# Kernel optimization log

Hardware: AMD Instinct MI355X
Metric: run time of the kernel (lower is better)

Reference implementation:

```python
import jax, jax.numpy as jnp
import numpy as np

TEMPERATURE = 0.5
EPS = 1e-8  # matches torch CosineSimilarity eps


def setup_inputs() -> dict:
    key = jax.random.key(0)
    k1, k2 = jax.random.split(key)
    N, D = 4096, 256
    z1 = jax.random.normal(k1, (N, D), dtype=jnp.float32)
    z2 = jax.random.normal(k2, (N, D), dtype=jnp.float32)
    return {"z1": z1, "z2": z2}


def reference(z1, z2):
    N = z1.shape[0]
    z = jnp.concatenate([z1, z2], axis=0)            # [2N, D]
    norm = jnp.linalg.norm(z, axis=-1, keepdims=True)
    zn = z / jnp.maximum(norm, EPS)                  # L2-normalized
    sim = (zn @ zn.T) / TEMPERATURE                  # [2N, 2N] cosine sim / temp
    # mask self-similarity on the diagonal
    diag = jnp.eye(2 * N, dtype=bool)
    sim = jnp.where(diag, -jnp.inf, sim)
    # positive pair labels: row i pairs with i+N (first half) or i-N (second half)
    labels = jnp.concatenate([jnp.arange(N) + N, jnp.arange(N)])
    logp = jax.nn.log_softmax(sim, axis=-1)
    loss = -jnp.mean(logp[jnp.arange(2 * N), labels])
    return loss
```

## Files before the change

### kernel.cpp

```cpp
#include <hip/hip_runtime.h>
#include <hip/hip_bf16.h>


#define NROWS 8192
#define NHALF 4096
#define DDIM  256

typedef __bf16 bf16;
typedef __bf16 bf16x4 __attribute__((ext_vector_type(4)));
typedef __bf16 bf16x8 __attribute__((ext_vector_type(8)));
typedef float  f32x4  __attribute__((ext_vector_type(4)));

__constant__ const float kTwoLog2e = 2.8853900817779268f;
__constant__ const float kLn2      = 0.6931471805599453f;

__device__ __forceinline__ const float* zrow(const float* z1, const float* z2, int r) {
  return (r < NHALF) ? (z1 + (size_t)r * DDIM) : (z2 + (size_t)(r - NHALF) * DDIM);
}

__global__ void k_normalize(const float* __restrict__ z1, const float* __restrict__ z2,
                            bf16* __restrict__ zn, float* __restrict__ invn,
                            float* __restrict__ rowsum) {
  const int wave = threadIdx.x >> 6, lane = threadIdx.x & 63;
  const int row = blockIdx.x * 4 + wave;
  const float* src = zrow(z1, z2, row);
  f32x4 v = *(const f32x4*)(src + lane * 4);
  float ss = v.x * v.x + v.y * v.y + v.z * v.z + v.w * v.w;
#pragma unroll
  for (int off = 1; off < 64; off <<= 1) ss += __shfl_xor(ss, off);
  const float inv = 1.0f / fmaxf(sqrtf(ss), 1e-8f);
  bf16x4 o;
  o.x = (bf16)(v.x * inv); o.y = (bf16)(v.y * inv);
  o.z = (bf16)(v.z * inv); o.w = (bf16)(v.w * inv);
  *(bf16x4*)(zn + (size_t)row * DDIM + lane * 4) = o;
  if (lane == 0) { invn[row] = inv; rowsum[row] = 0.0f; }
}

#define BM 256
#define BN 64
#define CSPLIT 8
#define LDSB 528

__global__ __launch_bounds__(512, 2) void k_gram(const bf16* __restrict__ zn,
                                                 float* __restrict__ rowsum) {
  __shared__ __align__(16) unsigned char lds[2][BN * LDSB];
  const int tid  = threadIdx.x;
  const int wave = tid >> 6, lane = tid & 63;
  const int quad = lane >> 4, l15 = lane & 15;
  const int rowblk = blockIdx.x >> 3, csplit = blockIdx.x & 7;
  const int c0 = csplit * (NROWS / CSPLIT);
  const int iters = (NROWS / CSPLIT) / BN;

  bf16x8 a[2][8];
#pragma unroll
  for (int s = 0; s < 2; ++s) {
    const int row = rowblk * BM + wave * 32 + s * 16 + l15;
    const bf16x8* ap = (const bf16x8*)(zn + (size_t)row * DDIM);
#pragma unroll
    for (int k = 0; k < 8; ++k) a[s][k] = ap[k * 4 + quad];
  }

  const int tr = tid >> 3;
  const int tc = tid & 7;

  uint4 g[4];
  {
    const unsigned char* gp = (const unsigned char*)(zn + (size_t)(c0 + tr) * DDIM);
#pragma unroll
    for (int j = 0; j < 4; ++j) g[j] = *(const uint4*)(gp + (tc + 8 * j) * 16);
  }
#pragma unroll
  for (int j = 0; j < 4; ++j)
    *(uint4*)(&lds[0][tr * LDSB + (tc + 8 * j) * 16]) = g[j];

  float sum[2][4] = {{0.f, 0.f, 0.f, 0.f}, {0.f, 0.f, 0.f, 0.f}};
  const f32x4 zero4 = {0.f, 0.f, 0.f, 0.f};

  for (int it = 0; it < iters; ++it) {
    __syncthreads();
    const int cur = it & 1;
    if (it + 1 < iters) {
      const unsigned char* gp =
          (const unsigned char*)(zn + (size_t)(c0 + (it + 1) * BN + tr) * DDIM);
#pragma unroll
      for (int j = 0; j < 4; ++j) g[j] = *(const uint4*)(gp + (tc + 8 * j) * 16);
    }

    f32x4 acc[2][4];
#pragma unroll
    for (int s = 0; s < 2; ++s)
#pragma unroll
      for (int cs = 0; cs < 4; ++cs) acc[s][cs] = zero4;

#pragma unroll
    for (int k = 0; k < 8; ++k) {
      bf16x8 b[4];
#pragma unroll
      for (int cs = 0; cs < 4; ++cs)
        b[cs] = *(const bf16x8*)(&lds[cur][(cs * 16 + l15) * LDSB + k * 64 + quad * 16]);
#pragma unroll
      for (int s = 0; s < 2; ++s)
#pragma unroll
        for (int cs = 0; cs < 4; ++cs)
          acc[s][cs] = __builtin_amdgcn_mfma_f32_16x16x32_bf16(a[s][k], b[cs], acc[s][cs], 0, 0, 0);
    }

#pragma unroll
    for (int s = 0; s < 2; ++s)
#pragma unroll
      for (int cs = 0; cs < 4; ++cs)
#pragma unroll
        for (int r = 0; r < 4; ++r)
          sum[s][r] += __builtin_amdgcn_exp2f(acc[s][cs][r] * kTwoLog2e);

    if (it + 1 < iters) {
#pragma unroll
      for (int j = 0; j < 4; ++j)
        *(uint4*)(&lds[(it + 1) & 1][tr * LDSB + (tc + 8 * j) * 16]) = g[j];
    }
  }

#pragma unroll
  for (int s = 0; s < 2; ++s)
#pragma unroll
    for (int r = 0; r < 4; ++r) {
      float v = sum[s][r];
      v += __shfl_xor(v, 1); v += __shfl_xor(v, 2);
      v += __shfl_xor(v, 4); v += __shfl_xor(v, 8);
      if (l15 == 0) {
        const int row = rowblk * BM + wave * 32 + s * 16 + quad * 4 + r;
        atomicAdd(&rowsum[row], v);
      }
    }
}

__global__ void k_finalize(const float* __restrict__ z1, const float* __restrict__ z2,
                           const bf16* __restrict__ zn, const float* __restrict__ invn,
                           const float* __restrict__ rowsum, float* __restrict__ contrib) {
  const int wave = threadIdx.x >> 6, lane = threadIdx.x & 63;
  const int row = blockIdx.x * 4 + wave;
  const int pr = (row < NHALF) ? row + NHALF : row - NHALF;

  f32x4 a4 = *(const f32x4*)(zrow(z1, z2, row) + lane * 4);
  f32x4 b4 = *(const f32x4*)(zrow(z1, z2, pr) + lane * 4);
  bf16x4 nb = *(const bf16x4*)(zn + (size_t)row * DDIM + lane * 4);

  float pd = a4.x * b4.x + a4.y * b4.y + a4.z * b4.z + a4.w * b4.w;
  float f0 = (float)nb.x, f1 = (float)nb.y, f2 = (float)nb.z, f3 = (float)nb.w;
  float nd = f0 * f0 + f1 * f1 + f2 * f2 + f3 * f3;
#pragma unroll
  for (int off = 1; off < 64; off <<= 1) {
    pd += __shfl_xor(pd, off);
    nd += __shfl_xor(nd, off);
  }
  if (lane == 0) {
    const float p = 2.0f * pd * invn[row] * invn[pr];
    const float dexp = __builtin_amdgcn_exp2f(kTwoLog2e * nd);
    const float lse = __builtin_amdgcn_logf(rowsum[row] - dexp) * kLn2;
    contrib[row] = lse - p;
  }
}

__global__ void k_reduce(const float* __restrict__ contrib, float* __restrict__ out) {
  const int wave = threadIdx.x >> 6, lane = threadIdx.x & 63;
  float acc = 0.0f;
  for (int i = threadIdx.x; i < NROWS; i += 256) acc += contrib[i];
#pragma unroll
  for (int off = 1; off < 64; off <<= 1) acc += __shfl_xor(acc, off);
  __shared__ float wsum[4];
  if (lane == 0) wsum[wave] = acc;
  __syncthreads();
  if (threadIdx.x == 0)
    out[0] = (wsum[0] + wsum[1] + wsum[2] + wsum[3]) * (1.0f / (float)NROWS);
}

extern "C" void kernel_launch(void* const* d_in, const int* in_sizes, int n_in,
                              void* d_out, int out_size, void* d_ws, size_t ws_size,
                              hipStream_t stream) {
  const float* z1 = (const float*)d_in[0];
  const float* z2 = (const float*)d_in[1];
  unsigned char* ws = (unsigned char*)d_ws;

  bf16* zn = (bf16*)ws;
  float* invn = (float*)(ws + (size_t)NROWS * DDIM * sizeof(bf16));
  float* rowsum = invn + NROWS;
  float* contrib = rowsum + NROWS;

  hipLaunchKernelGGL(k_normalize, dim3(NROWS / 4), dim3(256), 0, stream, z1, z2, zn, invn, rowsum);
  hipLaunchKernelGGL(k_gram, dim3((NROWS / BM) * CSPLIT), dim3(512), 0, stream, zn, rowsum);
  hipLaunchKernelGGL(k_finalize, dim3(NROWS / 4), dim3(256), 0, stream, z1, z2, zn, invn, rowsum,
                     contrib);
  hipLaunchKernelGGL(k_reduce, dim3(1), dim3(256), 0, stream, contrib, (float*)d_out);
}
```

Measured before the change: 107.6 us.

## Exploit Gram symmetry with upper-triangular tiles and fold temperature scaling into operands

The Gram kernel now computes only upper-triangular 128x128 tiles and adds each off-diagonal tile's exponentials into both the row sums and, through LDS column sums, the transposed row sums. That roughly halves the MFMA and exp work. The 2*log2e scale is folded into one bf16 copy of the normalized rows, which removes the per-element multiply. The finalize and reduce kernels are merged into one kernel that accumulates into the output with atomics, dropping a launch. In exchange, the positive-pair dot now uses the bf16 values instead of fp32, there is extra atomic traffic, and the triangular index decode is a serial loop.

```diff
diff --git a/kernel.cpp b/kernel.cpp
--- a/kernel.cpp
+++ b/kernel.cpp
@@ -5,85 +5,91 @@
 #define NROWS 8192
 #define NHALF 4096
 #define DDIM  256
+#define GT    128
+#define NTILES (NROWS / GT)
+#define NBLK  (NTILES * (NTILES + 1) / 2)
+#define BN    64
+#define LDSB  528
 
 typedef __bf16 bf16;
 typedef __bf16 bf16x4 __attribute__((ext_vector_type(4)));
 typedef __bf16 bf16x8 __attribute__((ext_vector_type(8)));
 typedef float  f32x4  __attribute__((ext_vector_type(4)));
 
-__constant__ const float kTwoLog2e = 2.8853900817779268f;
-__constant__ const float kLn2      = 0.6931471805599453f;
-
-__device__ __forceinline__ const float* zrow(const float* z1, const float* z2, int r) {
-  return (r < NHALF) ? (z1 + (size_t)r * DDIM) : (z2 + (size_t)(r - NHALF) * DDIM);
-}
+__constant__ const float kC   = 2.8853900817779268f;
+__constant__ const float kLn2 = 0.6931471805599453f;
 
 __global__ void k_normalize(const float* __restrict__ z1, const float* __restrict__ z2,
-                            bf16* __restrict__ zn, float* __restrict__ invn,
-                            float* __restrict__ rowsum) {
+                            bf16* __restrict__ znA, bf16* __restrict__ znB,
+                            float* __restrict__ rowsum, float* __restrict__ out) {
   const int wave = threadIdx.x >> 6, lane = threadIdx.x & 63;
   const int row = blockIdx.x * 4 + wave;
-  const float* src = zrow(z1, z2, row);
+  const float* src = (row < NHALF) ? z1 + (size_t)row * DDIM
+                                   : z2 + (size_t)(row - NHALF) * DDIM;
   f32x4 v = *(const f32x4*)(src + lane * 4);
   float ss = v.x * v.x + v.y * v.y + v.z * v.z + v.w * v.w;
 #pragma unroll
   for (int off = 1; off < 64; off <<= 1) ss += __shfl_xor(ss, off);
-  const float inv = 1.0f / fmaxf(sqrtf(ss), 1e-8f);
-  bf16x4 o;
-  o.x = (bf16)(v.x * inv); o.y = (bf16)(v.y * inv);
-  o.z = (bf16)(v.z * inv); o.w = (bf16)(v.w * inv);
-  *(bf16x4*)(zn + (size_t)row * DDIM + lane * 4) = o;
-  if (lane == 0) { invn[row] = inv; rowsum[row] = 0.0f; }
-}
-
-#define BM 256
-#define BN 64
-#define CSPLIT 8
-#define LDSB 528
-
-__global__ __launch_bounds__(512, 2) void k_gram(const bf16* __restrict__ zn,
+  const float inv  = 1.0f / fmaxf(sqrtf(ss), 1e-8f);
+  const float invc = inv * kC;
+  bf16x4 oa, ob;
+  oa.x = (bf16)(v.x * invc); oa.y = (bf16)(v.y * invc);
+  oa.z = (bf16)(v.z * invc); oa.w = (bf16)(v.w * invc);
+  ob.x = (bf16)(v.x * inv);  ob.y = (bf16)(v.y * inv);
+  ob.z = (bf16)(v.z * inv);  ob.w = (bf16)(v.w * inv);
+  *(bf16x4*)(znA + (size_t)row * DDIM + lane * 4) = oa;
+  *(bf16x4*)(znB + (size_t)row * DDIM + lane * 4) = ob;
+  if (lane == 0) rowsum[row] = 0.0f;
+  if (blockIdx.x == 0 && threadIdx.x == 0) out[0] = 0.0f;
+}
+
+__global__ __launch_bounds__(256, 2) void k_gram(const bf16* __restrict__ znA,
+                                                 const bf16* __restrict__ znB,
                                                  float* __restrict__ rowsum) {
   __shared__ __align__(16) unsigned char lds[2][BN * LDSB];
+  __shared__ float colsum[GT];
   const int tid  = threadIdx.x;
   const int wave = tid >> 6, lane = tid & 63;
   const int quad = lane >> 4, l15 = lane & 15;
-  const int rowblk = blockIdx.x >> 3, csplit = blockIdx.x & 7;
-  const int c0 = csplit * (NROWS / CSPLIT);
-  const int iters = (NROWS / CSPLIT) / BN;
+
+  int p = blockIdx.x, I = 0;
+  while (p >= NTILES - I) { p -= NTILES - I; ++I; }
+  const int J = I + p;
+  const bool diag = (I == J);
+  const int c0 = J * GT;
+
+  if (tid < GT) colsum[tid] = 0.0f;
 
   bf16x8 a[2][8];
 #pragma unroll
   for (int s = 0; s < 2; ++s) {
-    const int row = rowblk * BM + wave * 32 + s * 16 + l15;
-    const bf16x8* ap = (const bf16x8*)(zn + (size_t)row * DDIM);
+    const int row = I * GT + wave * 32 + s * 16 + l15;
+    const bf16x8* ap = (const bf16x8*)(znA + (size_t)row * DDIM);
 #pragma unroll
     for (int k = 0; k < 8; ++k) a[s][k] = ap[k * 4 + quad];
   }
 
-  const int tr = tid >> 3;
-  const int tc = tid & 7;
-
-  uint4 g[4];
+  const int tr = tid >> 2, tc = tid & 3;
+  uint4 g[8];
   {
-    const unsigned char* gp = (const unsigned char*)(zn + (size_t)(c0 + tr) * DDIM);
-#pragma unroll
-    for (int j = 0; j < 4; ++j) g[j] = *(const uint4*)(gp + (tc + 8 * j) * 16);
-  }
-#pragma unroll
-  for (int j = 0; j < 4; ++j)
-    *(uint4*)(&lds[0][tr * LDSB + (tc + 8 * j) * 16]) = g[j];
+    const unsigned char* gp = (const unsigned char*)(znB + (size_t)(c0 + tr) * DDIM);
+#pragma unroll
+    for (int j = 0; j < 8; ++j) g[j] = *(const uint4*)(gp + (tc + 4 * j) * 16);
+  }
+#pragma unroll
+  for (int j = 0; j < 8; ++j)
+    *(uint4*)(&lds[0][tr * LDSB + (tc + 4 * j) * 16]) = g[j];
 
   float sum[2][4] = {{0.f, 0.f, 0.f, 0.f}, {0.f, 0.f, 0.f, 0.f}};
   const f32x4 zero4 = {0.f, 0.f, 0.f, 0.f};
 
-  for (int it = 0; it < iters; ++it) {
+#pragma unroll
+  for (int it = 0; it < 2; ++it) {
     __syncthreads();
-    const int cur = it & 1;
-    if (it + 1 < iters) {
-      const unsigned char* gp =
-          (const unsigned char*)(zn + (size_t)(c0 + (it + 1) * BN + tr) * DDIM);
-#pragma unroll
-      for (int j = 0; j < 4; ++j) g[j] = *(const uint4*)(gp + (tc + 8 * j) * 16);
+    if (it == 0) {
+      const unsigned char* gp = (const unsigned char*)(znB + (size_t)(c0 + BN + tr) * DDIM);
+#pragma unroll
+      for (int j = 0; j < 8; ++j) g[j] = *(const uint4*)(gp + (tc + 4 * j) * 16);
     }
 
     f32x4 acc[2][4];
@@ -97,7 +103,7 @@
       bf16x8 b[4];
 #pragma unroll
       for (int cs = 0; cs < 4; ++cs)
-        b[cs] = *(const bf16x8*)(&lds[cur][(cs * 16 + l15) * LDSB + k * 64 + quad * 16]);
+        b[cs] = *(const bf16x8*)(&lds[it][(cs * 16 + l15) * LDSB + k * 64 + quad * 16]);
 #pragma unroll
       for (int s = 0; s < 2; ++s)
 #pragma unroll
@@ -105,18 +111,28 @@
           acc[s][cs] = __builtin_amdgcn_mfma_f32_16x16x32_bf16(a[s][k], b[cs], acc[s][cs], 0, 0, 0);
     }
 
-#pragma unroll
-    for (int s = 0; s < 2; ++s)
-#pragma unroll
-      for (int cs = 0; cs < 4; ++cs)
-#pragma unroll
-        for (int r = 0; r < 4; ++r)
-          sum[s][r] += __builtin_amdgcn_exp2f(acc[s][cs][r] * kTwoLog2e);
-
-    if (it + 1 < iters) {
-#pragma unroll
-      for (int j = 0; j < 4; ++j)
-        *(uint4*)(&lds[(it + 1) & 1][tr * LDSB + (tc + 8 * j) * 16]) = g[j];
+    if (it == 0) {
+#pragma unroll
+      for (int j = 0; j < 8; ++j)
+        *(uint4*)(&lds[1][tr * LDSB + (tc + 4 * j) * 16]) = g[j];
+    }
+
+#pragma unroll
+    for (int cs = 0; cs < 4; ++cs) {
+      float cp = 0.0f;
+#pragma unroll
+      for (int s = 0; s < 2; ++s)
+#pragma unroll
+        for (int r = 0; r < 4; ++r) {
+          const float v = __builtin_amdgcn_exp2f(acc[s][cs][r]);
+          sum[s][r] += v;
+          cp += v;
+        }
+      if (!diag) {
+        cp += __shfl_xor(cp, 16);
+        cp += __shfl_xor(cp, 32);
+        if (lane < 16) atomicAdd(&colsum[it * BN + cs * 16 + l15], cp);
+      }
     }
   }
 
@@ -127,51 +143,50 @@
       float v = sum[s][r];
       v += __shfl_xor(v, 1); v += __shfl_xor(v, 2);
       v += __shfl_xor(v, 4); v += __shfl_xor(v, 8);
-      if (l15 == 0) {
-        const int row = rowblk * BM + wave * 32 + s * 16 + quad * 4 + r;
-        atomicAdd(&rowsum[row], v);
-      }
-    }
-}
-
-__global__ void k_finalize(const float* __restrict__ z1, const float* __restrict__ z2,
-                           const bf16* __restrict__ zn, const float* __restrict__ invn,
-                           const float* __restrict__ rowsum, float* __restrict__ contrib) {
+      if (l15 == 0)
+        atomicAdd(&rowsum[I * GT + wave * 32 + s * 16 + quad * 4 + r], v);
+    }
+
+  __syncthreads();
+  if (!diag && tid < GT) atomicAdd(&rowsum[c0 + tid], colsum[tid]);
+}
+
+__device__ __forceinline__ float dot4(bf16x4 a, bf16x4 b) {
+  return (float)a.x * (float)b.x + (float)a.y * (float)b.y +
+         (float)a.z * (float)b.z + (float)a.w * (float)b.w;
+}
+
+__global__ void k_finalize(const bf16* __restrict__ znA, const bf16* __restrict__ znB,
+                           const float* __restrict__ rowsum, float* __restrict__ out) {
   const int wave = threadIdx.x >> 6, lane = threadIdx.x & 63;
-  const int row = blockIdx.x * 4 + wave;
-  const int pr = (row < NHALF) ? row + NHALF : row - NHALF;
-
-  f32x4 a4 = *(const f32x4*)(zrow(z1, z2, row) + lane * 4);
-  f32x4 b4 = *(const f32x4*)(zrow(z1, z2, pr) + lane * 4);
-  bf16x4 nb = *(const bf16x4*)(zn + (size_t)row * DDIM + lane * 4);
-
-  float pd = a4.x * b4.x + a4.y * b4.y + a4.z * b4.z + a4.w * b4.w;
-  float f0 = (float)nb.x, f1 = (float)nb.y, f2 = (float)nb.z, f3 = (float)nb.w;
-  float nd = f0 * f0 + f1 * f1 + f2 * f2 + f3 * f3;
-#pragma unroll
-  for (int off = 1; off < 64; off <<= 1) {
-    pd += __shfl_xor(pd, off);
-    nd += __shfl_xor(nd, off);
-  }
-  if (lane == 0) {
-    const float p = 2.0f * pd * invn[row] * invn[pr];
-    const float dexp = __builtin_amdgcn_exp2f(kTwoLog2e * nd);
-    const float lse = __builtin_amdgcn_logf(rowsum[row] - dexp) * kLn2;
-    contrib[row] = lse - p;
-  }
-}
-
-__global__ void k_reduce(const float* __restrict__ contrib, float* __restrict__ out) {
-  const int wave = threadIdx.x >> 6, lane = threadIdx.x & 63;
+  const int gw = blockIdx.x * 4 + wave;
   float acc = 0.0f;
-  for (int i = threadIdx.x; i < NROWS; i += 256) acc += contrib[i];
-#pragma unroll
-  for (int off = 1; off < 64; off <<= 1) acc += __shfl_xor(acc, off);
-  __shared__ float wsum[4];
-  if (lane == 0) wsum[wave] = acc;
+  for (int t = 0; t < 16; ++t) {
+    const int q = gw * 16 + t, pq = q + NHALF;
+    bf16x4 aq = *(const bf16x4*)(znA + (size_t)q  * DDIM + lane * 4);
+    bf16x4 bq = *(const bf16x4*)(znB + (size_t)q  * DDIM + lane * 4);
+    bf16x4 ap = *(const bf16x4*)(znA + (size_t)pq * DDIM + lane * 4);
+    bf16x4 bp = *(const bf16x4*)(znB + (size_t)pq * DDIM + lane * 4);
+    float dqq = dot4(aq, bq);
+    float dpp = dot4(ap, bp);
+    float dqp = dot4(aq, bp);
+#pragma unroll
+    for (int off = 1; off < 64; off <<= 1) {
+      dqq += __shfl_xor(dqq, off);
+      dpp += __shfl_xor(dpp, off);
+      dqp += __shfl_xor(dqp, off);
+    }
+    if (lane == 0) {
+      const float lseq = __builtin_amdgcn_logf(rowsum[q]  - __builtin_amdgcn_exp2f(dqq)) * kLn2;
+      const float lsep = __builtin_amdgcn_logf(rowsum[pq] - __builtin_amdgcn_exp2f(dpp)) * kLn2;
+      acc += lseq + lsep - 2.0f * dqp * kLn2;
+    }
+  }
+  __shared__ float ws4[4];
+  if (lane == 0) ws4[wave] = acc;
   __syncthreads();
   if (threadIdx.x == 0)
-    out[0] = (wsum[0] + wsum[1] + wsum[2] + wsum[3]) * (1.0f / (float)NROWS);
+    atomicAdd(out, (ws4[0] + ws4[1] + ws4[2] + ws4[3]) * (1.0f / (float)NROWS));
 }
 
 extern "C" void kernel_launch(void* const* d_in, const int* in_sizes, int n_in,
@@ -181,14 +196,12 @@
   const float* z2 = (const float*)d_in[1];
   unsigned char* ws = (unsigned char*)d_ws;
 
-  bf16* zn = (bf16*)ws;
-  float* invn = (float*)(ws + (size_t)NROWS * DDIM * sizeof(bf16));
-  float* rowsum = invn + NROWS;
-  float* contrib = rowsum + NROWS;
-
-  hipLaunchKernelGGL(k_normalize, dim3(NROWS / 4), dim3(256), 0, stream, z1, z2, zn, invn, rowsum);
-  hipLaunchKernelGGL(k_gram, dim3((NROWS / BM) * CSPLIT), dim3(512), 0, stream, zn, rowsum);
-  hipLaunchKernelGGL(k_finalize, dim3(NROWS / 4), dim3(256), 0, stream, z1, z2, zn, invn, rowsum,
-                     contrib);
-  hipLaunchKernelGGL(k_reduce, dim3(1), dim3(256), 0, stream, contrib, (float*)d_out);
-}
+  bf16* znA = (bf16*)ws;
+  bf16* znB = (bf16*)(ws + (size_t)NROWS * DDIM * sizeof(bf16));
+  float* rowsum = (float*)(ws + 2 * (size_t)NROWS * DDIM * sizeof(bf16));
+  float* out = (float*)d_out;
+
+  hipLaunchKernelGGL(k_normalize, dim3(NROWS / 4), dim3(256), 0, stream, z1, z2, znA, znB, rowsum, out);
+  hipLaunchKernelGGL(k_gram, dim3(NBLK), dim3(256), 0, stream, znA, znB, rowsum);
+  hipLaunchKernelGGL(k_finalize, dim3(64), dim3(256), 0, stream, znA, znB, rowsum, out);
+}
```

Result: slower. 128.3 us (+19.3%).
